# Kernel tuning notes

Hardware: AMD Instinct MI355X
Metric: run time of the kernel (lower is better)

The kernel has to match this reference:

```python
import jax, jax.numpy as jnp
import numpy as np
from jax import lax


def _binarize(t):
    # sign binarization to +1/-1 (zero maps to -1, matching torch.where(t > 0, 1, -1))
    return jnp.where(t > 0, 1.0, -1.0).astype(t.dtype)


def _bconv(x, w, b):
    # binary conv: binarize input and weights, then standard 3x3 'same' conv
    y = lax.conv_general_dilated(
        _binarize(x), _binarize(w),
        window_strides=(1, 1), padding=((1, 1), (1, 1)),
        dimension_numbers=('NCHW', 'OIHW', 'NCHW'))
    return y + b[None, :, None, None]


def _maxpool2(x):
    return lax.reduce_window(x, -jnp.inf, lax.max, (1, 1, 2, 2), (1, 1, 2, 2), 'VALID')


def setup_inputs() -> dict:
    key = jax.random.key(0)
    ks = jax.random.split(key, 13)
    s = 0.1
    return {
        'x': jax.random.normal(ks[0], (4096, 1, 28, 28), jnp.float32),
        'w1': jax.random.normal(ks[1], (32, 1, 3, 3), jnp.float32) * s,
        'b1': jax.random.normal(ks[2], (32,), jnp.float32) * s,
        'w2': jax.random.normal(ks[3], (64, 32, 3, 3), jnp.float32) * s,
        'b2': jax.random.normal(ks[4], (64,), jnp.float32) * s,
        'w3': jax.random.normal(ks[5], (16, 64, 3, 3), jnp.float32) * s,
        'b3': jax.random.normal(ks[6], (16,), jnp.float32) * s,
        'fc1_w': jax.random.normal(ks[7], (256, 16 * 7 * 7), jnp.float32) * s,
        'fc1_b': jax.random.normal(ks[8], (256,), jnp.float32) * s,
        'fc2_w': jax.random.normal(ks[9], (128, 256), jnp.float32) * s,
        'fc2_b': jax.random.normal(ks[10], (128,), jnp.float32) * s,
        'fc3_w': jax.random.normal(ks[11], (10, 128), jnp.float32) * s,
        'fc3_b': jax.random.normal(ks[12], (10,), jnp.float32) * s,
    }


def reference(x, w1, b1, w2, b2, w3, b3, fc1_w, fc1_b, fc2_w, fc2_b, fc3_w, fc3_b):
    h = jax.nn.relu(_maxpool2(_bconv(x, w1, b1)))      # [B,32,14,14]
    h = jax.nn.relu(_maxpool2(_bconv(h, w2, b2)))      # [B,64,7,7]
    h = jax.nn.relu(_bconv(h, w3, b3))                 # [B,16,7,7]
    h = h.reshape(-1, 16 * 7 * 7)
    h = jax.nn.relu(h @ fc1_w.T + fc1_b)
    h = jax.nn.relu(h @ fc2_w.T + fc2_b)
    return h @ fc3_w.T + fc3_b                          # [B,10]
```

## Files before the change

### kernel.cpp

```cpp
#include <hip/hip_runtime.h>
#include <cstdint>

#define OFF_PW    0
#define OFF_W1T   4096
#define OFF_W2T   823296
#define OFF_H3T   954368
#define OFF_H1T   14061568
#define OFF_H2T   18255872
#define OFF_H1EXT 20353024ull
#define OFF_H2EXT 32935936ull
#define WS_NEED_EXT 35033088ull

__global__ __launch_bounds__(256) void prep(
    const float* __restrict__ w1, const float* __restrict__ w2,
    const float* __restrict__ w3,
    const float* __restrict__ fc1_w, const float* __restrict__ fc2_w,
    uint32_t* __restrict__ pw, float* __restrict__ w1T,
    float* __restrict__ w2T, float* __restrict__ h3T) {
    int idx = blockIdx.x * 256 + threadIdx.x;
    if (idx < 204800) {
        int k = idx >> 8, n = idx & 255;
        w1T[idx] = (k < 784) ? fc1_w[n * 784 + k] : 0.f;
        return;
    }
    idx -= 204800;
    if (idx < 32768) {
        int k = idx >> 7, n = idx & 127;
        w2T[idx] = fc2_w[n * 256 + k];
        return;
    }
    idx -= 32768;
    if (idx < 65536) {
        h3T[784 * 4096 + idx] = 0.f;
        return;
    }
    idx -= 65536;
    if (idx >= 896) return;
    if (idx < 32) {
        uint32_t b = 0;
#pragma unroll
        for (int k = 0; k < 9; ++k) b |= (w1[idx * 9 + k] > 0.f ? 1u : 0u) << k;
        pw[idx] = b;
    } else if (idx < 608) {
        int e = idx - 32;
        int oc = e / 9, tap = e - oc * 9;
        uint32_t b = 0;
#pragma unroll
        for (int ic = 0; ic < 32; ++ic)
            b |= (w2[(oc * 32 + ic) * 9 + tap] > 0.f ? 1u : 0u) << ic;
        pw[idx] = b;
    } else {
        int e = idx - 608;
        int oc = e / 18, r = e - oc * 18;
        int tap = r >> 1, half = r & 1;
        uint32_t b = 0;
#pragma unroll
        for (int ic = 0; ic < 32; ++ic)
            b |= (w3[(oc * 64 + half * 32 + ic) * 9 + tap] > 0.f ? 1u : 0u) << ic;
        pw[idx] = b;
    }
}

__device__ __forceinline__ uint32_t bfe3(uint32_t r, int j) { return (r >> j) & 7u; }

__global__ __launch_bounds__(256, 4) void conv_stack(
    const float* __restrict__ x, const float* __restrict__ b1,
    const float* __restrict__ b2, const float* __restrict__ b3,
    const uint32_t* __restrict__ pw, float* __restrict__ h3T) {
    __shared__ __align__(16) uint32_t s_H1[4][16][16];
    __shared__ __align__(16) uint32_t s_H2[4][9][9][2];
    __shared__ uint32_t s_xr[4][32];
    __shared__ uint32_t s_w1[32];
    __shared__ int s_sth1[32], s_ic1[32], s_ic2[64];
    __shared__ uint32_t s_W2t[9][64];
    __shared__ uint32_t s_W3t[18][16];
    __shared__ float s_b3[16];

    const int t = threadIdx.x;
    const int lane = t & 63;
    const int wid = t >> 6;
    const int img0 = blockIdx.x * 4;

    {
        uint32_t* h1f = &s_H1[0][0][0];
        for (int i = t; i < 1024; i += 256) h1f[i] = 0;
        uint32_t* h2f = &s_H2[0][0][0][0];
        for (int i = t; i < 648; i += 256) h2f[i] = 0;
    }
    if (t < 32) {
        s_w1[t] = pw[t];
        int ic = (int)floorf(-b1[t]) + 1;
        s_ic1[t] = ic;
        s_sth1[t] = (9 - ic) >> 1;
    } else if (t < 96) {
        s_ic2[t - 32] = (int)floorf(-b2[t - 32]) + 1;
    } else if (t < 112) {
        s_b3[t - 96] = b3[t - 96];
    } else if (t >= 128 && t < 240) {
        int r = t - 128;
        int im = r / 28, row = r - im * 28;
        const float4* xr = (const float4*)(x + (img0 + im) * 784 + row * 28);
        uint32_t b = 0;
#pragma unroll
        for (int q = 0; q < 7; ++q) {
            float4 v = xr[q];
            b |= (v.x > 0.f ? 1u : 0u) << (q * 4 + 0);
            b |= (v.y > 0.f ? 1u : 0u) << (q * 4 + 1);
            b |= (v.z > 0.f ? 1u : 0u) << (q * 4 + 2);
            b |= (v.w > 0.f ? 1u : 0u) << (q * 4 + 3);
        }
        s_xr[im][row] = b << 1;
    }
    for (int i = t; i < 576; i += 256)
        s_W2t[i >> 6][i & 63] = pw[32 + (i & 63) * 9 + (i >> 6)];
    for (int i = t; i < 288; i += 256)
        s_W3t[i >> 4][i & 15] = pw[608 + (i & 15) * 18 + (i >> 4)];
    __syncthreads();

    for (int task = t; task < 784; task += 256) {
        int im = task & 3, pid = task >> 2;
        int pi, pj;
        if (pid < 144) { pi = 1 + pid / 12; pj = 1 + pid - (pid / 12) * 12; }
        else {
            int b = pid - 144;
            if (b < 14)      { pi = 0;  pj = b; }
            else if (b < 28) { pi = 13; pj = b - 14; }
            else if (b < 40) { pi = 1 + (b - 28); pj = 0; }
            else             { pi = 1 + (b - 40); pj = 13; }
        }
        const uint32_t* xr = &s_xr[im][0];
        int y0 = 2 * pi - 1;
        uint32_t r0 = (pi > 0)  ? xr[y0]     : 0u;
        uint32_t r1 = xr[y0 + 1];
        uint32_t r2 = xr[y0 + 2];
        uint32_t r3 = (pi < 13) ? xr[y0 + 3] : 0u;
        int j0 = 2 * pj, j1 = 2 * pj + 1;
        uint32_t s00 = bfe3(r0, j0) | (bfe3(r1, j0) << 3) | (bfe3(r2, j0) << 6);
        uint32_t s01 = bfe3(r0, j1) | (bfe3(r1, j1) << 3) | (bfe3(r2, j1) << 6);
        uint32_t s10 = bfe3(r1, j0) | (bfe3(r2, j0) << 3) | (bfe3(r3, j0) << 6);
        uint32_t s11 = bfe3(r1, j1) | (bfe3(r2, j1) << 3) | (bfe3(r3, j1) << 6);
        uint32_t word = 0;
        if (pid < 144) {
#pragma unroll 4
            for (int c = 0; c < 32; ++c) {
                uint32_t w = s_w1[c];
                int S = min(min(__popc(s00 ^ w), __popc(s01 ^ w)),
                            min(__popc(s10 ^ w), __popc(s11 ^ w)));
                word |= (uint32_t)(S <= s_sth1[c]) << c;
            }
        } else {
            uint32_t iT = (pi == 0)  ? 0x7u   : 0u;
            uint32_t iB = (pi == 13) ? 0x1C0u : 0u;
            uint32_t iL = (pj == 0)  ? 0x49u  : 0u;
            uint32_t iR = (pj == 13) ? 0x124u : 0u;
            uint32_t i00 = iT | iL, i01 = iT | iR, i10 = iB | iL, i11 = iB | iR;
            int n00 = 9 - __popc(i00), n01 = 9 - __popc(i01);
            int n10 = 9 - __popc(i10), n11 = 9 - __popc(i11);
#pragma unroll 4
            for (int c = 0; c < 32; ++c) {
                uint32_t w = s_w1[c];
                int v0 = n00 - 2 * (__popc(s00 ^ w) - __popc(w & i00));
                int v1 = n01 - 2 * (__popc(s01 ^ w) - __popc(w & i01));
                int v2 = n10 - 2 * (__popc(s10 ^ w) - __popc(w & i10));
                int v3 = n11 - 2 * (__popc(s11 ^ w) - __popc(w & i11));
                int vm = max(max(v0, v1), max(v2, v3));
                word |= (uint32_t)(vm >= s_ic1[c]) << c;
            }
        }
        s_H1[im][pi + 1][pj + 1] = word;
    }
    __syncthreads();

    {
        const int im = wid;
        uint32_t wv[9];
#pragma unroll
        for (int k = 0; k < 9; ++k) wv[k] = s_W2t[k][lane];
        int ic2 = s_ic2[lane];
        int sth2 = (288 - ic2) >> 1;
        int pc0 = __popc(wv[0]), pc2 = __popc(wv[2]);
        int pc6 = __popc(wv[6]), pc8 = __popc(wv[8]);
        int topc = pc0 + __popc(wv[1]) + pc2;
        int botc = pc6 + __popc(wv[7]) + pc8;
        int lefc = pc0 + __popc(wv[3]) + pc6;
        int rigc = pc2 + __popc(wv[5]) + pc8;
        const uint32_t* plane = &s_H1[im][0][0];

        for (int pi = 0; pi < 7; ++pi) {
            uint32_t C[4][16];
#pragma unroll
            for (int r = 0; r < 4; ++r) {
                const uint32_t* rp = &plane[(2 * pi + r) * 16];
                *(uint4*)&C[r][0]  = *(const uint4*)&rp[0];
                *(uint4*)&C[r][4]  = *(const uint4*)&rp[4];
                *(uint4*)&C[r][8]  = *(const uint4*)&rp[8];
                *(uint4*)&C[r][12] = *(const uint4*)&rp[12];
            }
            const int rT = (pi == 0), rB = (pi == 6);
#pragma unroll
            for (int pj = 0; pj < 7; ++pj) {
                int S00 = 0, S01 = 0, S10 = 0, S11 = 0;
#pragma unroll
                for (int kh = 0; kh < 3; ++kh)
#pragma unroll
                    for (int kw = 0; kw < 3; ++kw) {
                        uint32_t ww = wv[kh * 3 + kw];
                        S00 += __popc(C[kh][2 * pj + kw] ^ ww);
                        S01 += __popc(C[kh][2 * pj + 1 + kw] ^ ww);
                        S10 += __popc(C[kh + 1][2 * pj + kw] ^ ww);
                        S11 += __popc(C[kh + 1][2 * pj + 1 + kw] ^ ww);
                    }
                int pred;
                if (pj >= 1 && pj <= 5) {
                    if (!rT && !rB) {
                        int Sm = min(min(S00, S01), min(S10, S11));
                        pred = (Sm <= sth2);
                    } else if (rT) {
                        int v0 = 192 - 2 * (S00 - topc);
                        int v1 = 192 - 2 * (S01 - topc);
                        int v2 = 288 - 2 * S10;
                        int v3 = 288 - 2 * S11;
                        pred = (max(max(v0, v1), max(v2, v3)) >= ic2);
                    } else {
                        int v0 = 288 - 2 * S00;
                        int v1 = 288 - 2 * S01;
                        int v2 = 192 - 2 * (S10 - botc);
                        int v3 = 192 - 2 * (S11 - botc);
                        pred = (max(max(v0, v1), max(v2, v3)) >= ic2);
                    }
                } else {
                    const int cL = (pj == 0), cR = (pj == 6);
                    int v0, v1, v2, v3;
                    { int rI = rT, cI = cL;
                      int corr = (rI ? topc : 0) + (cI ? lefc : 0) - ((rI & cI) ? pc0 : 0);
                      int nv = 32 * (9 - 3 * rI - 3 * cI + (rI & cI));
                      v0 = nv - 2 * (S00 - corr); }
                    { int rI = rT, cI = cR;
                      int corr = (rI ? topc : 0) + (cI ? rigc : 0) - ((rI & cI) ? pc2 : 0);
                      int nv = 32 * (9 - 3 * rI - 3 * cI + (rI & cI));
                      v1 = nv - 2 * (S01 - corr); }
                    { int rI = rB, cI = cL;
                      int corr = (rI ? botc : 0) + (cI ? lefc : 0) - ((rI & cI) ? pc6 : 0);
                      int nv = 32 * (9 - 3 * rI - 3 * cI + (rI & cI));
                      v2 = nv - 2 * (S10 - corr); }
                    { int rI = rB, cI = cR;
                      int corr = (rI ? botc : 0) + (cI ? rigc : 0) - ((rI & cI) ? pc8 : 0);
                      int nv = 32 * (9 - 3 * rI - 3 * cI + (rI & cI));
                      v3 = nv - 2 * (S11 - corr); }
                    pred = (max(max(v0, v1), max(v2, v3)) >= ic2);
                }
                unsigned long long m = __ballot(pred);
                if (lane == 0)
                    *(uint2*)&s_H2[im][pi + 1][pj + 1][0] =
                        make_uint2((uint32_t)m, (uint32_t)(m >> 32));
            }
        }
    }
    __syncthreads();

    {
        int oc = lane & 15, im = lane >> 4;
        uint32_t w[18];
#pragma unroll
        for (int k = 0; k < 18; ++k) w[k] = s_W3t[k][oc];
        float bias3 = s_b3[oc];
        int pc[9];
#pragma unroll
        for (int k = 0; k < 9; ++k) pc[k] = __popc(w[2 * k]) + __popc(w[2 * k + 1]);
        int topc = pc[0] + pc[1] + pc[2], botc = pc[6] + pc[7] + pc[8];
        int lefc = pc[0] + pc[3] + pc[6], rigc = pc[2] + pc[5] + pc[8];

        for (int pos = wid; pos < 49; pos += 4) {
            int pi = pos / 7, pj = pos - pi * 7;
            int S = 0;
#pragma unroll
            for (int kh = 0; kh < 3; ++kh)
#pragma unroll
                for (int kw = 0; kw < 3; ++kw) {
                    uint2 cc = *(const uint2*)&s_H2[im][pi + kh][pj + kw][0];
                    int k = kh * 3 + kw;
                    S += __popc(cc.x ^ w[2 * k]) + __popc(cc.y ^ w[2 * k + 1]);
                }
            int v;
            if (pi >= 1 && pi <= 5 && pj >= 1 && pj <= 5) {
                v = 576 - 2 * S;
            } else {
                int rT = (pi == 0), rB = (pi == 6), cL = (pj == 0), cR = (pj == 6);
                int rA = rT | rB, cA = cL | cR;
                int corr = (rT ? topc : 0) + (rB ? botc : 0) +
                           (cL ? lefc : 0) + (cR ? rigc : 0);
                if (rT & cL) corr -= pc[0];
                if (rT & cR) corr -= pc[2];
                if (rB & cL) corr -= pc[6];
                if (rB & cR) corr -= pc[8];
                int nInv = 3 * rA + 3 * cA - (rA & cA);
                v = 64 * (9 - nInv) - 2 * (S - corr);
            }
            float h = fmaxf((float)v + bias3, 0.f);
            h3T[(oc * 49 + pos) * 4096 + img0 + im] = h;
        }
    }
}

__global__ __launch_bounds__(128, 2) void fc1_gemm(
    const float* __restrict__ aT, const float* __restrict__ bT,
    float* __restrict__ p0, float* __restrict__ pext, int bufmode) {
    __shared__ __align__(16) float As[40][64];
    __shared__ __align__(16) float Bs[40][128];
    const int t = threadIdx.x;
    const int img0 = blockIdx.x * 64;
    const int n0 = blockIdx.y * 128;
    const int z = blockIdx.z;
    const int k0 = z * 200;
    const int tx = t & 15, ty = t >> 4;
    float acc[8][8] = {{0.f}};

    for (int ch = 0; ch < 5; ++ch) {
        int kb = k0 + ch * 40;
#pragma unroll
        for (int s = 0; s < 5; ++s) {
            int fid = t + s * 128;
            int kk = fid >> 4, c4 = (fid & 15) * 4;
            *(float4*)&As[kk][c4] = *(const float4*)&aT[(kb + kk) * 4096 + img0 + c4];
        }
#pragma unroll
        for (int s = 0; s < 10; ++s) {
            int fid = t + s * 128;
            int kk = fid >> 5, c4 = (fid & 31) * 4;
            *(float4*)&Bs[kk][c4] = *(const float4*)&bT[(kb + kk) * 256 + n0 + c4];
        }
        __syncthreads();
#pragma unroll 4
        for (int kk = 0; kk < 40; ++kk) {
            float4 a0 = *(const float4*)&As[kk][ty * 8];
            float4 a1 = *(const float4*)&As[kk][ty * 8 + 4];
            float4 b0 = *(const float4*)&Bs[kk][tx * 8];
            float4 b1 = *(const float4*)&Bs[kk][tx * 8 + 4];
            float av[8] = {a0.x, a0.y, a0.z, a0.w, a1.x, a1.y, a1.z, a1.w};
            float bv[8] = {b0.x, b0.y, b0.z, b0.w, b1.x, b1.y, b1.z, b1.w};
#pragma unroll
            for (int i = 0; i < 8; ++i)
#pragma unroll
                for (int j = 0; j < 8; ++j) acc[i][j] += av[i] * bv[j];
        }
        __syncthreads();
    }
    if (bufmode) {
        float* dst = (z == 0) ? p0 : pext + (size_t)(z - 1) * 1048576;
#pragma unroll
        for (int j = 0; j < 8; ++j) {
            float* d = &dst[(n0 + tx * 8 + j) * 4096 + img0 + ty * 8];
            float4 v0 = make_float4(acc[0][j], acc[1][j], acc[2][j], acc[3][j]);
            float4 v1 = make_float4(acc[4][j], acc[5][j], acc[6][j], acc[7][j]);
            *(float4*)&d[0] = v0;
            *(float4*)&d[4] = v1;
        }
    } else {
#pragma unroll
        for (int j = 0; j < 8; ++j) {
            float* d = &p0[(n0 + tx * 8 + j) * 4096 + img0 + ty * 8];
#pragma unroll
            for (int i = 0; i < 8; ++i) atomicAdd(&d[i], acc[i][j]);
        }
    }
}

__global__ __launch_bounds__(256, 2) void fc2_gemm(
    const float* __restrict__ p0, const float* __restrict__ pext,
    const float* __restrict__ fc1_b,
    const float* __restrict__ bT,
    float* __restrict__ q0, float* __restrict__ qext, int bufmode) {
    __shared__ __align__(16) float As[32][64];
    __shared__ __align__(16) float Bs[32][64];
    const int t = threadIdx.x;
    const int img0 = blockIdx.x * 64;
    const int n0 = blockIdx.y * 64;
    const int z = blockIdx.z;
    const int k0 = z * 128;
    const int tx = t & 15, ty = t >> 4;
    float acc[4][4] = {{0.f}};

    for (int ch = 0; ch < 4; ++ch) {
        int kb = k0 + ch * 32;
        {
            int kk = t >> 3, c4 = (t & 7) * 8;
            size_t off = (size_t)(kb + kk) * 4096 + img0 + c4;
            float4 v0 = *(const float4*)&p0[off];
            float4 v1 = *(const float4*)&p0[off + 4];
            if (bufmode) {
#pragma unroll
                for (int s = 0; s < 3; ++s) {
                    const float* pp = pext + (size_t)s * 1048576;
                    float4 u0 = *(const float4*)&pp[off];
                    float4 u1 = *(const float4*)&pp[off + 4];
                    v0.x += u0.x; v0.y += u0.y; v0.z += u0.z; v0.w += u0.w;
                    v1.x += u1.x; v1.y += u1.y; v1.z += u1.z; v1.w += u1.w;
                }
            }
            float bb = fc1_b[kb + kk];
            v0.x = fmaxf(v0.x + bb, 0.f); v0.y = fmaxf(v0.y + bb, 0.f);
            v0.z = fmaxf(v0.z + bb, 0.f); v0.w = fmaxf(v0.w + bb, 0.f);
            v1.x = fmaxf(v1.x + bb, 0.f); v1.y = fmaxf(v1.y + bb, 0.f);
            v1.z = fmaxf(v1.z + bb, 0.f); v1.w = fmaxf(v1.w + bb, 0.f);
            *(float4*)&As[kk][c4] = v0;
            *(float4*)&As[kk][c4 + 4] = v1;
            *(float4*)&Bs[kk][c4] = *(const float4*)&bT[(kb + kk) * 128 + n0 + c4];
            *(float4*)&Bs[kk][c4 + 4] = *(const float4*)&bT[(kb + kk) * 128 + n0 + c4 + 4];
        }
        __syncthreads();
#pragma unroll 8
        for (int kk = 0; kk < 32; ++kk) {
            float4 a = *(const float4*)&As[kk][ty * 4];
            float4 b = *(const float4*)&Bs[kk][tx * 4];
            float av[4] = {a.x, a.y, a.z, a.w};
            float bv[4] = {b.x, b.y, b.z, b.w};
#pragma unroll
            for (int i = 0; i < 4; ++i)
#pragma unroll
                for (int j = 0; j < 4; ++j) acc[i][j] += av[i] * bv[j];
        }
        __syncthreads();
    }
    if (bufmode) {
        float* dst = (z == 0) ? q0 : qext;
#pragma unroll
        for (int j = 0; j < 4; ++j) {
            float4 v = make_float4(acc[0][j], acc[1][j], acc[2][j], acc[3][j]);
            *(float4*)&dst[(n0 + tx * 4 + j) * 4096 + img0 + ty * 4] = v;
        }
    } else {
#pragma unroll
        for (int j = 0; j < 4; ++j) {
            float* d = &q0[(n0 + tx * 4 + j) * 4096 + img0 + ty * 4];
#pragma unroll
            for (int i = 0; i < 4; ++i) atomicAdd(&d[i], acc[i][j]);
        }
    }
}

__global__ __launch_bounds__(256) void fc3_gemm(
    const float* __restrict__ q0, const float* __restrict__ qext,
    const float* __restrict__ fc2_b,
    const float* __restrict__ w, const float* __restrict__ bias,
    float* __restrict__ out, int bufmode) {
    int id = blockIdx.x * 256 + threadIdx.x;
    int n = id >> 12, img = id & 4095;
    const float* wr = w + n * 128;
    float a0 = 0.f, a1 = 0.f;
#pragma unroll 8
    for (int k = 0; k < 128; k += 2) {
        float v0 = q0[(k + 0) * 4096 + img];
        float v1 = q0[(k + 1) * 4096 + img];
        if (bufmode) {
            v0 += qext[(k + 0) * 4096 + img];
            v1 += qext[(k + 1) * 4096 + img];
        }
        v0 = fmaxf(v0 + fc2_b[k], 0.f);
        v1 = fmaxf(v1 + fc2_b[k + 1], 0.f);
        a0 += v0 * wr[k];
        a1 += v1 * wr[k + 1];
    }
    out[img * 10 + n] = a0 + a1 + bias[n];
}

extern "C" void kernel_launch(void* const* d_in, const int* in_sizes, int n_in,
                              void* d_out, int out_size, void* d_ws, size_t ws_size,
                              hipStream_t stream) {
    const float* x     = (const float*)d_in[0];
    const float* w1    = (const float*)d_in[1];
    const float* b1    = (const float*)d_in[2];
    const float* w2    = (const float*)d_in[3];
    const float* b2    = (const float*)d_in[4];
    const float* w3    = (const float*)d_in[5];
    const float* b3    = (const float*)d_in[6];
    const float* fc1_w = (const float*)d_in[7];
    const float* fc1_b = (const float*)d_in[8];
    const float* fc2_w = (const float*)d_in[9];
    const float* fc2_b = (const float*)d_in[10];
    const float* fc3_w = (const float*)d_in[11];
    const float* fc3_b = (const float*)d_in[12];
    float* out = (float*)d_out;

    const int B = in_sizes[0] / 784;
    char* ws = (char*)d_ws;
    uint32_t* pw = (uint32_t*)(ws + OFF_PW);
    float* w1T = (float*)(ws + OFF_W1T);
    float* w2T = (float*)(ws + OFF_W2T);
    float* h3T = (float*)(ws + OFF_H3T);
    float* h1p0 = (float*)(ws + OFF_H1T);
    float* h2p0 = (float*)(ws + OFF_H2T);
    const int bufmode = (ws_size >= WS_NEED_EXT) ? 1 : 0;
    float* h1ext = bufmode ? (float*)(ws + OFF_H1EXT) : h1p0;
    float* h2ext = bufmode ? (float*)(ws + OFF_H2EXT) : h2p0;

    if (!bufmode) {
        hipMemsetAsync(h1p0, 0, 4194304, stream);
        hipMemsetAsync(h2p0, 0, 2097152, stream);
    }
    hipLaunchKernelGGL(prep, dim3(1188), dim3(256), 0, stream,
                       w1, w2, w3, fc1_w, fc2_w, pw, w1T, w2T, h3T);
    hipLaunchKernelGGL(conv_stack, dim3(B / 4), dim3(256), 0, stream,
                       x, b1, b2, b3, pw, h3T);
    hipLaunchKernelGGL(fc1_gemm, dim3(B / 64, 2, 4), dim3(128), 0, stream,
                       h3T, w1T, h1p0, h1ext, bufmode);
    hipLaunchKernelGGL(fc2_gemm, dim3(B / 64, 2, 2), dim3(256), 0, stream,
                       h1p0, h1ext, fc1_b, w2T, h2p0, h2ext, bufmode);
    hipLaunchKernelGGL(fc3_gemm, dim3(B * 10 / 256), dim3(256), 0, stream,
                       h2p0, h2ext, fc2_b, fc3_w, fc3_b, out, bufmode);
}
```

Measured before the change: 224.4 us.

## Fuse FC layers into one kernel and fold weight prep into conv

Removes the separate prep kernel by having conv_stack binarize conv weights straight into shared memory and transpose the FC weights to the workspace as a side task. The three split-K FC GEMM kernels and their partial-sum buffers are replaced by a single fc_stack kernel. In it, each 16-image block runs fc1, fc2 and fc3 back to back, keeping activations in shared memory. This cuts kernel launches, memsets and the global round trips of intermediate activations. In exchange, every block re-reads the full fc1 weight matrix from L2, and the fused kernel runs only 256 blocks at low occupancy with small per-thread register tiles.

```diff
diff --git a/kernel.cpp b/kernel.cpp
--- a/kernel.cpp
+++ b/kernel.cpp
@@ -1,72 +1,20 @@
 #include <hip/hip_runtime.h>
 #include <cstdint>
 
-#define OFF_PW    0
-#define OFF_W1T   4096
-#define OFF_W2T   823296
-#define OFF_H3T   954368
-#define OFF_H1T   14061568
-#define OFF_H2T   18255872
-#define OFF_H1EXT 20353024ull
-#define OFF_H2EXT 32935936ull
-#define WS_NEED_EXT 35033088ull
-
-__global__ __launch_bounds__(256) void prep(
+#define OFF_W1T   0
+#define OFF_W2T   802816
+#define OFF_H3T   933888
+
+__device__ __forceinline__ uint32_t bfe3(uint32_t r, int j) { return (r >> j) & 7u; }
+
+__global__ __launch_bounds__(256, 4) void conv_stack(
+    const float* __restrict__ x, const float* __restrict__ b1,
+    const float* __restrict__ b2, const float* __restrict__ b3,
     const float* __restrict__ w1, const float* __restrict__ w2,
     const float* __restrict__ w3,
     const float* __restrict__ fc1_w, const float* __restrict__ fc2_w,
-    uint32_t* __restrict__ pw, float* __restrict__ w1T,
-    float* __restrict__ w2T, float* __restrict__ h3T) {
-    int idx = blockIdx.x * 256 + threadIdx.x;
-    if (idx < 204800) {
-        int k = idx >> 8, n = idx & 255;
-        w1T[idx] = (k < 784) ? fc1_w[n * 784 + k] : 0.f;
-        return;
-    }
-    idx -= 204800;
-    if (idx < 32768) {
-        int k = idx >> 7, n = idx & 127;
-        w2T[idx] = fc2_w[n * 256 + k];
-        return;
-    }
-    idx -= 32768;
-    if (idx < 65536) {
-        h3T[784 * 4096 + idx] = 0.f;
-        return;
-    }
-    idx -= 65536;
-    if (idx >= 896) return;
-    if (idx < 32) {
-        uint32_t b = 0;
-#pragma unroll
-        for (int k = 0; k < 9; ++k) b |= (w1[idx * 9 + k] > 0.f ? 1u : 0u) << k;
-        pw[idx] = b;
-    } else if (idx < 608) {
-        int e = idx - 32;
-        int oc = e / 9, tap = e - oc * 9;
-        uint32_t b = 0;
-#pragma unroll
-        for (int ic = 0; ic < 32; ++ic)
-            b |= (w2[(oc * 32 + ic) * 9 + tap] > 0.f ? 1u : 0u) << ic;
-        pw[idx] = b;
-    } else {
-        int e = idx - 608;
-        int oc = e / 18, r = e - oc * 18;
-        int tap = r >> 1, half = r & 1;
-        uint32_t b = 0;
-#pragma unroll
-        for (int ic = 0; ic < 32; ++ic)
-            b |= (w3[(oc * 64 + half * 32 + ic) * 9 + tap] > 0.f ? 1u : 0u) << ic;
-        pw[idx] = b;
-    }
-}
-
-__device__ __forceinline__ uint32_t bfe3(uint32_t r, int j) { return (r >> j) & 7u; }
-
-__global__ __launch_bounds__(256, 4) void conv_stack(
-    const float* __restrict__ x, const float* __restrict__ b1,
-    const float* __restrict__ b2, const float* __restrict__ b3,
-    const uint32_t* __restrict__ pw, float* __restrict__ h3T) {
+    float* __restrict__ w1T, float* __restrict__ w2T,
+    float* __restrict__ h3T) {
     __shared__ __align__(16) uint32_t s_H1[4][16][16];
     __shared__ __align__(16) uint32_t s_H2[4][9][9][2];
     __shared__ uint32_t s_xr[4][32];
@@ -82,13 +30,28 @@
     const int img0 = blockIdx.x * 4;
 
     {
+        int e = blockIdx.x * 256 + t;
+        if (e < 200704) {
+            int k = e >> 8, n = e & 255;
+            w1T[e] = fc1_w[n * 784 + k];
+        } else if (e < 233472) {
+            int e2 = e - 200704;
+            int k = e2 >> 7, n = e2 & 127;
+            w2T[e2] = fc2_w[n * 256 + k];
+        }
+    }
+
+    {
         uint32_t* h1f = &s_H1[0][0][0];
         for (int i = t; i < 1024; i += 256) h1f[i] = 0;
         uint32_t* h2f = &s_H2[0][0][0][0];
         for (int i = t; i < 648; i += 256) h2f[i] = 0;
     }
     if (t < 32) {
-        s_w1[t] = pw[t];
+        uint32_t b = 0;
+#pragma unroll
+        for (int k = 0; k < 9; ++k) b |= (w1[t * 9 + k] > 0.f ? 1u : 0u) << k;
+        s_w1[t] = b;
         int ic = (int)floorf(-b1[t]) + 1;
         s_ic1[t] = ic;
         s_sth1[t] = (9 - ic) >> 1;
@@ -111,10 +74,25 @@
         }
         s_xr[im][row] = b << 1;
     }
-    for (int i = t; i < 576; i += 256)
-        s_W2t[i >> 6][i & 63] = pw[32 + (i & 63) * 9 + (i >> 6)];
-    for (int i = t; i < 288; i += 256)
-        s_W3t[i >> 4][i & 15] = pw[608 + (i & 15) * 18 + (i >> 4)];
+    for (int i = t; i < 576; i += 256) {
+        int tap = i >> 6, oc = i & 63;
+        const float* wp = w2 + oc * 288 + tap;
+        uint32_t b = 0;
+#pragma unroll
+        for (int ic = 0; ic < 32; ++ic)
+            b |= (wp[ic * 9] > 0.f ? 1u : 0u) << ic;
+        s_W2t[tap][oc] = b;
+    }
+    for (int i = t; i < 288; i += 256) {
+        int w18 = i >> 4, oc = i & 15;
+        int tap = w18 >> 1, half = w18 & 1;
+        const float* wp = w3 + oc * 576 + half * 288 + tap;
+        uint32_t b = 0;
+#pragma unroll
+        for (int ic = 0; ic < 32; ++ic)
+            b |= (wp[ic * 9] > 0.f ? 1u : 0u) << ic;
+        s_W3t[w18][oc] = b;
+    }
     __syncthreads();
 
     for (int task = t; task < 784; task += 256) {
@@ -302,165 +280,103 @@
     }
 }
 
-__global__ __launch_bounds__(128, 2) void fc1_gemm(
-    const float* __restrict__ aT, const float* __restrict__ bT,
-    float* __restrict__ p0, float* __restrict__ pext, int bufmode) {
-    __shared__ __align__(16) float As[40][64];
-    __shared__ __align__(16) float Bs[40][128];
+__global__ __launch_bounds__(256, 1) void fc_stack(
+    const float* __restrict__ h3T, const float* __restrict__ w1T,
+    const float* __restrict__ fc1_b,
+    const float* __restrict__ w2T, const float* __restrict__ fc2_b,
+    const float* __restrict__ fc3_w, const float* __restrict__ fc3_b,
+    float* __restrict__ out) {
+    __shared__ __align__(16) float s_h[12544];
     const int t = threadIdx.x;
-    const int img0 = blockIdx.x * 64;
-    const int n0 = blockIdx.y * 128;
-    const int z = blockIdx.z;
-    const int k0 = z * 200;
-    const int tx = t & 15, ty = t >> 4;
-    float acc[8][8] = {{0.f}};
-
-    for (int ch = 0; ch < 5; ++ch) {
-        int kb = k0 + ch * 40;
-#pragma unroll
-        for (int s = 0; s < 5; ++s) {
-            int fid = t + s * 128;
-            int kk = fid >> 4, c4 = (fid & 15) * 4;
-            *(float4*)&As[kk][c4] = *(const float4*)&aT[(kb + kk) * 4096 + img0 + c4];
-        }
-#pragma unroll
-        for (int s = 0; s < 10; ++s) {
-            int fid = t + s * 128;
-            int kk = fid >> 5, c4 = (fid & 31) * 4;
-            *(float4*)&Bs[kk][c4] = *(const float4*)&bT[(kb + kk) * 256 + n0 + c4];
-        }
-        __syncthreads();
-#pragma unroll 4
-        for (int kk = 0; kk < 40; ++kk) {
-            float4 a0 = *(const float4*)&As[kk][ty * 8];
-            float4 a1 = *(const float4*)&As[kk][ty * 8 + 4];
-            float4 b0 = *(const float4*)&Bs[kk][tx * 8];
-            float4 b1 = *(const float4*)&Bs[kk][tx * 8 + 4];
-            float av[8] = {a0.x, a0.y, a0.z, a0.w, a1.x, a1.y, a1.z, a1.w};
-            float bv[8] = {b0.x, b0.y, b0.z, b0.w, b1.x, b1.y, b1.z, b1.w};
-#pragma unroll
-            for (int i = 0; i < 8; ++i)
-#pragma unroll
-                for (int j = 0; j < 8; ++j) acc[i][j] += av[i] * bv[j];
-        }
-        __syncthreads();
-    }
-    if (bufmode) {
-        float* dst = (z == 0) ? p0 : pext + (size_t)(z - 1) * 1048576;
-#pragma unroll
-        for (int j = 0; j < 8; ++j) {
-            float* d = &dst[(n0 + tx * 8 + j) * 4096 + img0 + ty * 8];
-            float4 v0 = make_float4(acc[0][j], acc[1][j], acc[2][j], acc[3][j]);
-            float4 v1 = make_float4(acc[4][j], acc[5][j], acc[6][j], acc[7][j]);
-            *(float4*)&d[0] = v0;
-            *(float4*)&d[4] = v1;
-        }
-    } else {
-#pragma unroll
-        for (int j = 0; j < 8; ++j) {
-            float* d = &p0[(n0 + tx * 8 + j) * 4096 + img0 + ty * 8];
-#pragma unroll
-            for (int i = 0; i < 8; ++i) atomicAdd(&d[i], acc[i][j]);
-        }
-    }
-}
-
-__global__ __launch_bounds__(256, 2) void fc2_gemm(
-    const float* __restrict__ p0, const float* __restrict__ pext,
-    const float* __restrict__ fc1_b,
-    const float* __restrict__ bT,
-    float* __restrict__ q0, float* __restrict__ qext, int bufmode) {
-    __shared__ __align__(16) float As[32][64];
-    __shared__ __align__(16) float Bs[32][64];
-    const int t = threadIdx.x;
-    const int img0 = blockIdx.x * 64;
-    const int n0 = blockIdx.y * 64;
-    const int z = blockIdx.z;
-    const int k0 = z * 128;
-    const int tx = t & 15, ty = t >> 4;
+    const int lane = t & 63, wv = t >> 6;
+    const int ng = lane & 15, ig = lane >> 4;
+    const int img0 = blockIdx.x * 16;
+
+    for (int f = t; f < 3136; f += 256) {
+        int k = f >> 2, q = (f & 3) * 4;
+        *(float4*)&s_h[k * 16 + q] = *(const float4*)&h3T[k * 4096 + img0 + q];
+    }
+    __syncthreads();
+
     float acc[4][4] = {{0.f}};
-
-    for (int ch = 0; ch < 4; ++ch) {
-        int kb = k0 + ch * 32;
-        {
-            int kk = t >> 3, c4 = (t & 7) * 8;
-            size_t off = (size_t)(kb + kk) * 4096 + img0 + c4;
-            float4 v0 = *(const float4*)&p0[off];
-            float4 v1 = *(const float4*)&p0[off + 4];
-            if (bufmode) {
-#pragma unroll
-                for (int s = 0; s < 3; ++s) {
-                    const float* pp = pext + (size_t)s * 1048576;
-                    float4 u0 = *(const float4*)&pp[off];
-                    float4 u1 = *(const float4*)&pp[off + 4];
-                    v0.x += u0.x; v0.y += u0.y; v0.z += u0.z; v0.w += u0.w;
-                    v1.x += u1.x; v1.y += u1.y; v1.z += u1.z; v1.w += u1.w;
-                }
-            }
-            float bb = fc1_b[kb + kk];
-            v0.x = fmaxf(v0.x + bb, 0.f); v0.y = fmaxf(v0.y + bb, 0.f);
-            v0.z = fmaxf(v0.z + bb, 0.f); v0.w = fmaxf(v0.w + bb, 0.f);
-            v1.x = fmaxf(v1.x + bb, 0.f); v1.y = fmaxf(v1.y + bb, 0.f);
-            v1.z = fmaxf(v1.z + bb, 0.f); v1.w = fmaxf(v1.w + bb, 0.f);
-            *(float4*)&As[kk][c4] = v0;
-            *(float4*)&As[kk][c4 + 4] = v1;
-            *(float4*)&Bs[kk][c4] = *(const float4*)&bT[(kb + kk) * 128 + n0 + c4];
-            *(float4*)&Bs[kk][c4 + 4] = *(const float4*)&bT[(kb + kk) * 128 + n0 + c4 + 4];
-        }
-        __syncthreads();
+    {
+        const int n0 = wv * 64 + ng * 4;
+        const float* bp = w1T + n0;
+        const float* ap = s_h + ig * 4;
 #pragma unroll 8
-        for (int kk = 0; kk < 32; ++kk) {
-            float4 a = *(const float4*)&As[kk][ty * 4];
-            float4 b = *(const float4*)&Bs[kk][tx * 4];
-            float av[4] = {a.x, a.y, a.z, a.w};
-            float bv[4] = {b.x, b.y, b.z, b.w};
-#pragma unroll
-            for (int i = 0; i < 4; ++i)
-#pragma unroll
-                for (int j = 0; j < 4; ++j) acc[i][j] += av[i] * bv[j];
-        }
-        __syncthreads();
-    }
-    if (bufmode) {
-        float* dst = (z == 0) ? q0 : qext;
-#pragma unroll
-        for (int j = 0; j < 4; ++j) {
-            float4 v = make_float4(acc[0][j], acc[1][j], acc[2][j], acc[3][j]);
-            *(float4*)&dst[(n0 + tx * 4 + j) * 4096 + img0 + ty * 4] = v;
-        }
-    } else {
-#pragma unroll
-        for (int j = 0; j < 4; ++j) {
-            float* d = &q0[(n0 + tx * 4 + j) * 4096 + img0 + ty * 4];
-#pragma unroll
-            for (int i = 0; i < 4; ++i) atomicAdd(&d[i], acc[i][j]);
-        }
-    }
-}
-
-__global__ __launch_bounds__(256) void fc3_gemm(
-    const float* __restrict__ q0, const float* __restrict__ qext,
-    const float* __restrict__ fc2_b,
-    const float* __restrict__ w, const float* __restrict__ bias,
-    float* __restrict__ out, int bufmode) {
-    int id = blockIdx.x * 256 + threadIdx.x;
-    int n = id >> 12, img = id & 4095;
-    const float* wr = w + n * 128;
-    float a0 = 0.f, a1 = 0.f;
+        for (int k = 0; k < 784; ++k) {
+            float4 b = *(const float4*)&bp[k * 256];
+            float4 a = *(const float4*)&ap[k * 16];
+            acc[0][0] += a.x * b.x; acc[0][1] += a.x * b.y;
+            acc[0][2] += a.x * b.z; acc[0][3] += a.x * b.w;
+            acc[1][0] += a.y * b.x; acc[1][1] += a.y * b.y;
+            acc[1][2] += a.y * b.z; acc[1][3] += a.y * b.w;
+            acc[2][0] += a.z * b.x; acc[2][1] += a.z * b.y;
+            acc[2][2] += a.z * b.z; acc[2][3] += a.z * b.w;
+            acc[3][0] += a.w * b.x; acc[3][1] += a.w * b.y;
+            acc[3][2] += a.w * b.z; acc[3][3] += a.w * b.w;
+        }
+    }
+    __syncthreads();
+    {
+        const int n0 = wv * 64 + ng * 4;
+#pragma unroll
+        for (int jj = 0; jj < 4; ++jj) {
+            float bb = fc1_b[n0 + jj];
+            float4 v;
+            v.x = fmaxf(acc[0][jj] + bb, 0.f);
+            v.y = fmaxf(acc[1][jj] + bb, 0.f);
+            v.z = fmaxf(acc[2][jj] + bb, 0.f);
+            v.w = fmaxf(acc[3][jj] + bb, 0.f);
+            *(float4*)&s_h[(n0 + jj) * 16 + ig * 4] = v;
+        }
+    }
+    __syncthreads();
+
+    float ac2[4][2] = {{0.f}};
+    {
+        const int n0 = wv * 32 + ng * 2;
+        const float* bp = w2T + n0;
+        const float* ap = s_h + ig * 4;
 #pragma unroll 8
-    for (int k = 0; k < 128; k += 2) {
-        float v0 = q0[(k + 0) * 4096 + img];
-        float v1 = q0[(k + 1) * 4096 + img];
-        if (bufmode) {
-            v0 += qext[(k + 0) * 4096 + img];
-            v1 += qext[(k + 1) * 4096 + img];
-        }
-        v0 = fmaxf(v0 + fc2_b[k], 0.f);
-        v1 = fmaxf(v1 + fc2_b[k + 1], 0.f);
-        a0 += v0 * wr[k];
-        a1 += v1 * wr[k + 1];
-    }
-    out[img * 10 + n] = a0 + a1 + bias[n];
+        for (int k = 0; k < 256; ++k) {
+            float2 b = *(const float2*)&bp[k * 128];
+            float4 a = *(const float4*)&ap[k * 16];
+            ac2[0][0] += a.x * b.x; ac2[0][1] += a.x * b.y;
+            ac2[1][0] += a.y * b.x; ac2[1][1] += a.y * b.y;
+            ac2[2][0] += a.z * b.x; ac2[2][1] += a.z * b.y;
+            ac2[3][0] += a.w * b.x; ac2[3][1] += a.w * b.y;
+        }
+    }
+    {
+        const int n0 = wv * 32 + ng * 2;
+#pragma unroll
+        for (int jj = 0; jj < 2; ++jj) {
+            float bb = fc2_b[n0 + jj];
+            float4 v;
+            v.x = fmaxf(ac2[0][jj] + bb, 0.f);
+            v.y = fmaxf(ac2[1][jj] + bb, 0.f);
+            v.z = fmaxf(ac2[2][jj] + bb, 0.f);
+            v.w = fmaxf(ac2[3][jj] + bb, 0.f);
+            *(float4*)&s_h[4096 + (n0 + jj) * 16 + ig * 4] = v;
+        }
+    }
+    __syncthreads();
+
+    if (t < 160) {
+        int img = t / 10, n = t - (t / 10) * 10;
+        const float* wr = fc3_w + n * 128;
+        const float* hp = s_h + 4096 + img;
+        float a0 = 0.f, a1 = 0.f, a2 = 0.f, a3 = 0.f;
+#pragma unroll 8
+        for (int k = 0; k < 128; k += 4) {
+            a0 += hp[(k + 0) * 16] * wr[k + 0];
+            a1 += hp[(k + 1) * 16] * wr[k + 1];
+            a2 += hp[(k + 2) * 16] * wr[k + 2];
+            a3 += hp[(k + 3) * 16] * wr[k + 3];
+        }
+        out[(img0 + img) * 10 + n] = (a0 + a1) + (a2 + a3) + fc3_b[n];
+    }
 }
 
 extern "C" void kernel_launch(void* const* d_in, const int* in_sizes, int n_in,
@@ -483,28 +399,12 @@
 
     const int B = in_sizes[0] / 784;
     char* ws = (char*)d_ws;
-    uint32_t* pw = (uint32_t*)(ws + OFF_PW);
     float* w1T = (float*)(ws + OFF_W1T);
     float* w2T = (float*)(ws + OFF_W2T);
     float* h3T = (float*)(ws + OFF_H3T);
-    float* h1p0 = (float*)(ws + OFF_H1T);
-    float* h2p0 = (float*)(ws + OFF_H2T);
-    const int bufmode = (ws_size >= WS_NEED_EXT) ? 1 : 0;
-    float* h1ext = bufmode ? (float*)(ws + OFF_H1EXT) : h1p0;
-    float* h2ext = bufmode ? (float*)(ws + OFF_H2EXT) : h2p0;
-
-    if (!bufmode) {
-        hipMemsetAsync(h1p0, 0, 4194304, stream);
-        hipMemsetAsync(h2p0, 0, 2097152, stream);
-    }
-    hipLaunchKernelGGL(prep, dim3(1188), dim3(256), 0, stream,
-                       w1, w2, w3, fc1_w, fc2_w, pw, w1T, w2T, h3T);
+
     hipLaunchKernelGGL(conv_stack, dim3(B / 4), dim3(256), 0, stream,
-                       x, b1, b2, b3, pw, h3T);
-    hipLaunchKernelGGL(fc1_gemm, dim3(B / 64, 2, 4), dim3(128), 0, stream,
-                       h3T, w1T, h1p0, h1ext, bufmode);
-    hipLaunchKernelGGL(fc2_gemm, dim3(B / 64, 2, 2), dim3(256), 0, stream,
-                       h1p0, h1ext, fc1_b, w2T, h2p0, h2ext, bufmode);
-    hipLaunchKernelGGL(fc3_gemm, dim3(B * 10 / 256), dim3(256), 0, stream,
-                       h2p0, h2ext, fc2_b, fc3_w, fc3_b, out, bufmode);
+                       x, b1, b2, b3, w1, w2, w3, fc1_w, fc2_w, w1T, w2T, h3T);
+    hipLaunchKernelGGL(fc_stack, dim3(B / 16), dim3(256), 0, stream,
+                       h3T, w1T, fc1_b, w2T, fc2_b, fc3_w, fc3_b, out);
 }
```

Result: slower. 243.6 us (+8.6%).
